# Performance work log

Hardware: AMD Instinct MI355X
Metric: run time of the kernel (lower is better)

## Reference

```python
import jax, jax.numpy as jnp
import numpy as np

EMB = 1024
HEAD = 64

def setup_inputs() -> dict:
    key = jax.random.key(0)
    ks = jax.random.split(key, 7)
    s = 1.0 / np.sqrt(EMB)
    x = jax.random.normal(ks[0], (4, 2048, EMB), dtype=jnp.float32)
    Wq = jax.random.uniform(ks[1], (EMB, HEAD), jnp.float32, -s, s)
    bq = jax.random.uniform(ks[2], (HEAD,), jnp.float32, -s, s)
    Wk = jax.random.uniform(ks[3], (EMB, HEAD), jnp.float32, -s, s)
    bk = jax.random.uniform(ks[4], (HEAD,), jnp.float32, -s, s)
    Wv = jax.random.uniform(ks[5], (EMB, HEAD), jnp.float32, -s, s)
    bv = jax.random.uniform(ks[6], (HEAD,), jnp.float32, -s, s)
    return {"x": x, "Wq": Wq, "bq": bq, "Wk": Wk, "bk": bk, "Wv": Wv, "bv": bv}

def reference(x, Wq, bq, Wk, bk, Wv, bv):
    x = x.astype(jnp.float32)
    q = jnp.einsum('bse,ed->bsd', x, Wq) + bq  # [B,S,H]
    k = jnp.einsum('bse,ed->bsd', x, Wk) + bk
    v = jnp.einsum('bse,ed->bsd', x, Wv) + bv
    scale = 1.0 / jnp.sqrt(jnp.asarray(k.shape[-1], jnp.float32))
    scores = jnp.einsum('bqd,bkd->bqk', q, k) * scale  # [B,S,S]
    attn = jax.nn.softmax(scores, axis=-1)
    return jnp.einsum('bqk,bkd->bqd', attn, v)  # [B,S,H]
```

## Files before the change

kernel.cpp:

```cpp
#include <hip/hip_runtime.h>
#include <hip/hip_bf16.h>

#define ROWS_TOTAL 8192
#define EMB 1024
#define HEAD 64
#define SEQ 2048
#define KSPLIT 8
#define KC (SEQ / KSPLIT)
#define KT 64

typedef __attribute__((ext_vector_type(8))) short short8;
typedef __attribute__((ext_vector_type(4))) float f32x4;

#define MFMA16(a, b, c) __builtin_amdgcn_mfma_f32_16x16x32_bf16((a), (b), (c), 0, 0, 0)

static __device__ __forceinline__ unsigned short f2bf(float f) {
    union { float f; unsigned u; } v; v.f = f;
    unsigned r = v.u + 0x7fff + ((v.u >> 16) & 1);
    return (unsigned short)(r >> 16);
}

static __device__ __forceinline__ unsigned pk2(float a, float b) {
    __hip_bfloat162 h = __float22bfloat162_rn(float2{a, b});
    union { __hip_bfloat162 h; unsigned u; } v; v.h = h;
    return v.u;
}

__global__ __launch_bounds__(256) void wprep_kernel(
    const float* __restrict__ Wq, const float* __restrict__ Wk,
    const float* __restrict__ Wv, unsigned short* __restrict__ Wt)
{
    __shared__ float Tr[64][65];
    const int m  = blockIdx.y;
    const int k0 = blockIdx.x * 64;
    const float* __restrict__ W = (m == 0) ? Wq : (m == 1) ? Wk : Wv;
    const int t = threadIdx.x;

    #pragma unroll
    for (int j = 0; j < 4; ++j) {
        int flat = j * 1024 + t * 4;
        int k = flat >> 6, n = flat & 63;
        float4 w4 = *(const float4*)&W[(size_t)(k0 + k) * 64 + n];
        Tr[n + 0][k] = w4.x; Tr[n + 1][k] = w4.y;
        Tr[n + 2][k] = w4.z; Tr[n + 3][k] = w4.w;
    }
    __syncthreads();

    const int n  = t >> 2;
    const int kc = (t & 3) * 16;
    union { short8 s; unsigned u[4]; } o0, o1;
    #pragma unroll
    for (int i = 0; i < 4; ++i) {
        o0.u[i] = pk2(Tr[n][kc + 2 * i],     Tr[n][kc + 2 * i + 1]);
        o1.u[i] = pk2(Tr[n][kc + 8 + 2 * i], Tr[n][kc + 9 + 2 * i]);
    }
    unsigned short* dst = &Wt[((size_t)m * 64 + n) * 1024 + k0 + kc];
    *(short8*)(dst)     = o0.s;
    *(short8*)(dst + 8) = o1.s;
}

__global__ __launch_bounds__(512) void qkv_mfma(
    const float* __restrict__ x, const unsigned short* __restrict__ Wt,
    const float* __restrict__ bq, const float* __restrict__ bk,
    const float* __restrict__ bv,
    unsigned short* __restrict__ Qb, unsigned short* __restrict__ Kb,
    unsigned short* __restrict__ Vt)
{
    __shared__ f32x4 pr[4][3][64];
    __shared__ unsigned short vlds[64][20];

    const int t    = threadIdx.x;
    const int w    = t >> 6;
    const int lane = t & 63;
    const int ln   = lane & 15;
    const int quad = lane >> 4;
    const int m0   = blockIdx.x * 16;
    const int cg   = w >> 1;
    const int kh   = w & 1;

    const f32x4 zero = (f32x4){0.f, 0.f, 0.f, 0.f};
    f32x4 acc[3];
    #pragma unroll
    for (int j = 0; j < 3; ++j) acc[j] = zero;

    const float* __restrict__ xrow = x + (size_t)(m0 + ln) * EMB + kh * 512;
    const unsigned short* __restrict__ wbase =
        Wt + (size_t)(cg * 48 + ln) * 1024 + kh * 512 + quad * 8;

    #pragma unroll 2
    for (int kc = 0; kc < 512; kc += 32) {
        float4 a0 = *(const float4*)&xrow[kc + quad * 8];
        float4 a1 = *(const float4*)&xrow[kc + quad * 8 + 4];
        union { short8 s; unsigned u[4]; } af;
        af.u[0] = pk2(a0.x, a0.y);
        af.u[1] = pk2(a0.z, a0.w);
        af.u[2] = pk2(a1.x, a1.y);
        af.u[3] = pk2(a1.z, a1.w);
        #pragma unroll
        for (int j = 0; j < 3; ++j) {
            short8 bf = *(const short8*)&wbase[(size_t)j * 16 * 1024 + kc];
            acc[j] = MFMA16(af.s, bf, acc[j]);
        }
    }

    if (kh == 1) {
        #pragma unroll
        for (int j = 0; j < 3; ++j) pr[cg][j][lane] = acc[j];
    }
    __syncthreads();

    if (kh == 0) {
        const float qs = 0.125f * 1.44269504f;
        #pragma unroll
        for (int j = 0; j < 3; ++j) {
            acc[j] += pr[cg][j][lane];
            const int tile = cg * 3 + j;
            const int mat  = tile >> 2;
            const int d    = (tile & 3) * 16 + ln;
            const float* bp = (mat == 0) ? bq : (mat == 1) ? bk : bv;
            const float bias = bp[d];
            #pragma unroll
            for (int r = 0; r < 4; ++r) {
                float vfull = acc[j][r] + bias;
                int row = m0 + quad * 4 + r;
                if (mat == 0)      Qb[(size_t)row * 64 + d] = f2bf(vfull * qs);
                else if (mat == 1) Kb[(size_t)row * 64 + d] = f2bf(vfull);
                else               vlds[d][quad * 4 + r] = f2bf(vfull);
            }
        }
    }
    __syncthreads();

    if (t < 256) {
        const int b  = m0 >> 11;
        const int s0 = m0 & 2047;
        const int d  = t >> 2;
        const int sq = (t & 3) * 4;
        ushort4 pk = {vlds[d][sq + 0], vlds[d][sq + 1],
                      vlds[d][sq + 2], vlds[d][sq + 3]};
        *(ushort4*)&Vt[((size_t)b * 64 + d) * SEQ + s0 + sq] = pk;
    }
}

__global__ __launch_bounds__(512) void attn_mfma(
    const unsigned short* __restrict__ Qb, const unsigned short* __restrict__ Kb,
    const unsigned short* __restrict__ Vt,
    float* __restrict__ Opart, float* __restrict__ lpart)
{
    __shared__ unsigned short Kl[KT][72];
    __shared__ unsigned short Vl[HEAD][72];
    __shared__ unsigned short Plds[8][16][72];

    const int t    = threadIdx.x;
    const int w    = t >> 6;
    const int lane = t & 63;
    const int ln   = lane & 15;
    const int quad = lane >> 4;

    const int c  = blockIdx.y;
    const int q0 = blockIdx.x * 128 + w * 16;
    const int b  = blockIdx.x >> 4;

    const unsigned short* qbase = Qb + (size_t)(q0 + ln) * 64 + quad * 8;
    short8 qa0 = *(const short8*)(qbase);
    short8 qa1 = *(const short8*)(qbase + 32);

    const f32x4 zero = (f32x4){0.f, 0.f, 0.f, 0.f};
    f32x4 O[4];
    #pragma unroll
    for (int j = 0; j < 4; ++j) O[j] = zero;
    float lacc[4] = {0.f, 0.f, 0.f, 0.f};

    const int skey = t >> 3;
    const int soff = (t & 7) * 8;
    const unsigned short* Ksrc =
        Kb + ((size_t)b * SEQ + c * KC + skey) * 64 + soff;
    const unsigned short* Vsrc =
        Vt + ((size_t)b * 64 + skey) * SEQ + c * KC + soff;

    unsigned short* P = &Plds[w][0][0];

    for (int kt = 0; kt < KC; kt += KT) {
        *(short8*)&Kl[skey][soff] = *(const short8*)(Ksrc + (size_t)kt * 64);
        *(short8*)&Vl[skey][soff] = *(const short8*)(Vsrc + kt);
        __syncthreads();

        f32x4 s[4];
        #pragma unroll
        for (int sub = 0; sub < 4; ++sub) {
            short8 kb0 = *(const short8*)&Kl[sub * 16 + ln][quad * 8];
            short8 kb1 = *(const short8*)&Kl[sub * 16 + ln][32 + quad * 8];
            s[sub] = MFMA16(qa0, kb0, zero);
            s[sub] = MFMA16(qa1, kb1, s[sub]);
        }

        #pragma unroll
        for (int r = 0; r < 4; ++r) {
            float p0 = __builtin_amdgcn_exp2f(s[0][r]);
            float p1 = __builtin_amdgcn_exp2f(s[1][r]);
            float p2 = __builtin_amdgcn_exp2f(s[2][r]);
            float p3 = __builtin_amdgcn_exp2f(s[3][r]);
            lacc[r] += (p0 + p1) + (p2 + p3);
            unsigned u01 = pk2(p0, p1);
            unsigned u23 = pk2(p2, p3);
            unsigned short* prow = P + (quad * 4 + r) * 72;
            prow[ln]      = (unsigned short)u01;
            prow[16 + ln] = (unsigned short)(u01 >> 16);
            prow[32 + ln] = (unsigned short)u23;
            prow[48 + ln] = (unsigned short)(u23 >> 16);
        }
        short8 pa0 = *(const short8*)&Plds[w][ln][quad * 8];
        short8 pa1 = *(const short8*)&Plds[w][ln][32 + quad * 8];

        #pragma unroll
        for (int j = 0; j < 4; ++j) {
            short8 vb0 = *(const short8*)&Vl[j * 16 + ln][quad * 8];
            short8 vb1 = *(const short8*)&Vl[j * 16 + ln][32 + quad * 8];
            O[j] = MFMA16(pa0, vb0, O[j]);
            O[j] = MFMA16(pa1, vb1, O[j]);
        }
        __syncthreads();
    }

    #pragma unroll
    for (int m = 1; m < 16; m <<= 1) {
        #pragma unroll
        for (int r = 0; r < 4; ++r) lacc[r] += __shfl_xor(lacc[r], m);
    }

    float* __restrict__ ob = Opart + ((size_t)c * ROWS_TOTAL + q0) * 64;
    #pragma unroll
    for (int j = 0; j < 4; ++j)
        #pragma unroll
        for (int r = 0; r < 4; ++r)
            ob[(size_t)(quad * 4 + r) * 64 + j * 16 + ln] = O[j][r];

    if (ln == 0) {
        #pragma unroll
        for (int r = 0; r < 4; ++r)
            lpart[(size_t)c * ROWS_TOTAL + q0 + quad * 4 + r] = lacc[r];
    }
}

__global__ __launch_bounds__(256) void reduce_kernel(
    const float* __restrict__ Opart, const float* __restrict__ lpart,
    float* __restrict__ out)
{
    const int idx = blockIdx.x * 256 + threadIdx.x;
    const int r   = idx >> 6;
    float osum = 0.f, lsum = 0.f;
    #pragma unroll
    for (int c = 0; c < KSPLIT; ++c) {
        osum += Opart[(size_t)c * ROWS_TOTAL * HEAD + idx];
        lsum += lpart[(size_t)c * ROWS_TOTAL + r];
    }
    out[idx] = osum / lsum;
}

extern "C" void kernel_launch(void* const* d_in, const int* in_sizes, int n_in,
                              void* d_out, int out_size, void* d_ws, size_t ws_size,
                              hipStream_t stream)
{
    const float* x  = (const float*)d_in[0];
    const float* Wq = (const float*)d_in[1];
    const float* bq = (const float*)d_in[2];
    const float* Wk = (const float*)d_in[3];
    const float* bk = (const float*)d_in[4];
    const float* Wv = (const float*)d_in[5];
    const float* bv = (const float*)d_in[6];
    float* out = (float*)d_out;

    char* ws = (char*)d_ws;
    unsigned short* Qb = (unsigned short*)ws;
    unsigned short* Kb = Qb + (size_t)ROWS_TOTAL * HEAD;
    unsigned short* Vt = Kb + (size_t)ROWS_TOTAL * HEAD;
    unsigned short* Wt = Vt + (size_t)ROWS_TOTAL * HEAD;
    float* lpart = (float*)(Wt + (size_t)3 * HEAD * EMB);
    float* Opart = lpart + (size_t)KSPLIT * ROWS_TOTAL;

    wprep_kernel<<<dim3(16, 3), 256, 0, stream>>>(Wq, Wk, Wv, Wt);
    qkv_mfma<<<dim3(512), 512, 0, stream>>>(x, Wt, bq, bk, bv, Qb, Kb, Vt);
    attn_mfma<<<dim3(64, KSPLIT), 512, 0, stream>>>(Qb, Kb, Vt, Opart, lpart);
    reduce_kernel<<<dim3((ROWS_TOTAL * HEAD) / 256), 256, 0, stream>>>(Opart, lpart, out);
}
```

Measured before the change: 134.9 us.

## Pre-tile weights in MFMA fragment order and stage x through LDS in QKV projection

The weight prep kernel now writes bf16 weights in a fragment-major layout ([k32 chunk][tile][lane row][32]), so each wave's B-fragment loads are contiguous 1KB blocks instead of strided rows. The QKV projection kernel now loads x cooperatively with coalesced float4 reads, converts it to bf16 once and stores it in a shared tile. Waves then read A fragments from LDS, which removes the redundant per-wave global x loads and conversions. In exchange it adds two barriers per 128-wide K step and drops the previous unroll-2 software overlap.

```diff
diff --git a/kernel.cpp b/kernel.cpp
--- a/kernel.cpp
+++ b/kernel.cpp
@@ -28,7 +28,7 @@
 
 __global__ __launch_bounds__(256) void wprep_kernel(
     const float* __restrict__ Wq, const float* __restrict__ Wk,
-    const float* __restrict__ Wv, unsigned short* __restrict__ Wt)
+    const float* __restrict__ Wv, unsigned short* __restrict__ Wf)
 {
     __shared__ float Tr[64][65];
     const int m  = blockIdx.y;
@@ -46,26 +46,31 @@
     }
     __syncthreads();
 
-    const int n  = t >> 2;
-    const int kc = (t & 3) * 16;
+    const int n   = t >> 2;
+    const int k16 = t & 3;
     union { short8 s; unsigned u[4]; } o0, o1;
     #pragma unroll
     for (int i = 0; i < 4; ++i) {
-        o0.u[i] = pk2(Tr[n][kc + 2 * i],     Tr[n][kc + 2 * i + 1]);
-        o1.u[i] = pk2(Tr[n][kc + 8 + 2 * i], Tr[n][kc + 9 + 2 * i]);
-    }
-    unsigned short* dst = &Wt[((size_t)m * 64 + n) * 1024 + k0 + kc];
-    *(short8*)(dst)     = o0.s;
-    *(short8*)(dst + 8) = o1.s;
+        o0.u[i] = pk2(Tr[n][k16 * 16 + 2 * i],     Tr[n][k16 * 16 + 2 * i + 1]);
+        o1.u[i] = pk2(Tr[n][k16 * 16 + 8 + 2 * i], Tr[n][k16 * 16 + 9 + 2 * i]);
+    }
+    const int tile = m * 4 + (n >> 4);
+    const int ln   = n & 15;
+    const int kc32 = (k0 >> 5) + (k16 >> 1);
+    const int half = k16 & 1;
+    size_t off = ((size_t)(kc32 * 12 + tile) * 16 + ln) * 32 + half * 16;
+    *(short8*)&Wf[off]     = o0.s;
+    *(short8*)&Wf[off + 8] = o1.s;
 }
 
 __global__ __launch_bounds__(512) void qkv_mfma(
-    const float* __restrict__ x, const unsigned short* __restrict__ Wt,
+    const float* __restrict__ x, const unsigned short* __restrict__ Wf,
     const float* __restrict__ bq, const float* __restrict__ bk,
     const float* __restrict__ bv,
     unsigned short* __restrict__ Qb, unsigned short* __restrict__ Kb,
     unsigned short* __restrict__ Vt)
 {
+    __shared__ unsigned short Xl[16][136];
     __shared__ f32x4 pr[4][3][64];
     __shared__ unsigned short vlds[64][20];
 
@@ -83,24 +88,30 @@
     #pragma unroll
     for (int j = 0; j < 3; ++j) acc[j] = zero;
 
-    const float* __restrict__ xrow = x + (size_t)(m0 + ln) * EMB + kh * 512;
-    const unsigned short* __restrict__ wbase =
-        Wt + (size_t)(cg * 48 + ln) * 1024 + kh * 512 + quad * 8;
-
-    #pragma unroll 2
-    for (int kc = 0; kc < 512; kc += 32) {
-        float4 a0 = *(const float4*)&xrow[kc + quad * 8];
-        float4 a1 = *(const float4*)&xrow[kc + quad * 8 + 4];
-        union { short8 s; unsigned u[4]; } af;
-        af.u[0] = pk2(a0.x, a0.y);
-        af.u[1] = pk2(a0.z, a0.w);
-        af.u[2] = pk2(a1.x, a1.y);
-        af.u[3] = pk2(a1.z, a1.w);
-        #pragma unroll
-        for (int j = 0; j < 3; ++j) {
-            short8 bf = *(const short8*)&wbase[(size_t)j * 16 * 1024 + kc];
-            acc[j] = MFMA16(af.s, bf, acc[j]);
-        }
+    const int srow = t >> 5;
+    const int scol = (t & 31) * 4;
+    const float* __restrict__ xsrc = x + (size_t)(m0 + srow) * EMB + scol;
+
+    for (int kt = 0; kt < EMB; kt += 128) {
+        float4 xv = *(const float4*)(xsrc + kt);
+        uint2 pk; pk.x = pk2(xv.x, xv.y); pk.y = pk2(xv.z, xv.w);
+        *(uint2*)&Xl[srow][scol] = pk;
+        __syncthreads();
+
+        #pragma unroll
+        for (int cc = 0; cc < 2; ++cc) {
+            short8 af = *(const short8*)&Xl[ln][kh * 64 + cc * 32 + quad * 8];
+            const int kc32 = (kt >> 5) + kh * 2 + cc;
+            #pragma unroll
+            for (int j = 0; j < 3; ++j) {
+                const int tile = cg * 3 + j;
+                const unsigned short* wp =
+                    Wf + ((size_t)(kc32 * 12 + tile) * 16 + ln) * 32 + quad * 8;
+                short8 bf = *(const short8*)wp;
+                acc[j] = MFMA16(af, bf, acc[j]);
+            }
+        }
+        __syncthreads();
     }
 
     if (kh == 1) {
@@ -274,12 +285,12 @@
     unsigned short* Qb = (unsigned short*)ws;
     unsigned short* Kb = Qb + (size_t)ROWS_TOTAL * HEAD;
     unsigned short* Vt = Kb + (size_t)ROWS_TOTAL * HEAD;
-    unsigned short* Wt = Vt + (size_t)ROWS_TOTAL * HEAD;
-    float* lpart = (float*)(Wt + (size_t)3 * HEAD * EMB);
+    unsigned short* Wf = Vt + (size_t)ROWS_TOTAL * HEAD;
+    float* lpart = (float*)(Wf + (size_t)3 * HEAD * EMB);
     float* Opart = lpart + (size_t)KSPLIT * ROWS_TOTAL;
 
-    wprep_kernel<<<dim3(16, 3), 256, 0, stream>>>(Wq, Wk, Wv, Wt);
-    qkv_mfma<<<dim3(512), 512, 0, stream>>>(x, Wt, bq, bk, bv, Qb, Kb, Vt);
+    wprep_kernel<<<dim3(16, 3), 256, 0, stream>>>(Wq, Wk, Wv, Wf);
+    qkv_mfma<<<dim3(512), 512, 0, stream>>>(x, Wf, bq, bk, bv, Qb, Kb, Vt);
     attn_mfma<<<dim3(64, KSPLIT), 512, 0, stream>>>(Qb, Kb, Vt, Opart, lpart);
     reduce_kernel<<<dim3((ROWS_TOTAL * HEAD) / 256), 256, 0, stream>>>(Opart, lpart, out);
 }
```

Measured after the change: 118.8 us. -11.9%, faster.
